# Performance work log

Measured on AMD Instinct MI355X. Metric: run time of the kernel, lower is better.

## Reference

```python
import jax, jax.numpy as jnp
import numpy as np

N = 5000        # nodes
F = 7699        # node feature dim (fixed by code)
E = 40000       # edges
ED = 3          # edge_dim (fixed by code)
H1, C1 = 4, 1024
H2, C2 = 1, 1024
NUM_OUT = 128
NEG_SLOPE = 0.2


def _glorot(key, shape):
    fan_in = shape[0]
    return jax.random.normal(key, shape, jnp.float32) / np.float32(np.sqrt(fan_in))


def setup_inputs() -> dict:
    key = jax.random.key(0)
    ks = jax.random.split(key, 16)
    x = jax.random.normal(ks[0], (N, F), jnp.float32)
    src = jax.random.randint(ks[1], (E,), 0, N)
    dst = jax.random.randint(ks[2], (E,), 0, N)
    src = jnp.where(src == dst, (src + 1) % N, src)  # no pre-existing self loops
    edge_index = jnp.stack([src, dst]).astype(jnp.int32)
    edge_attr = jax.random.normal(ks[3], (E, ED), jnp.float32)
    inp = {
        "x": x, "edge_index": edge_index, "edge_attr": edge_attr,
        # GATv2Conv #1: 7699 -> 1024, heads=4, edge_dim=3
        "W1l": _glorot(ks[4], (F, H1 * C1)), "b1l": jnp.zeros((H1 * C1,), jnp.float32),
        "W1r": _glorot(ks[5], (F, H1 * C1)), "b1r": jnp.zeros((H1 * C1,), jnp.float32),
        "W1e": _glorot(ks[6], (ED, H1 * C1)),
        "att1": _glorot(ks[7], (H1, C1)),
        "bias1": jnp.zeros((H1 * C1,), jnp.float32),
        # GATv2Conv #2: 4096 -> 1024, heads=1, edge_dim=3
        "W2l": _glorot(ks[8], (H1 * C1, H2 * C2)), "b2l": jnp.zeros((H2 * C2,), jnp.float32),
        "W2r": _glorot(ks[9], (H1 * C1, H2 * C2)), "b2r": jnp.zeros((H2 * C2,), jnp.float32),
        "W2e": _glorot(ks[10], (ED, H2 * C2)),
        "att2": _glorot(ks[11], (H2, C2)),
        "bias2": jnp.zeros((H2 * C2,), jnp.float32),
        # final Linear(1024, num_outputs)
        "Wlin": _glorot(ks[12], (C2, NUM_OUT)), "blin": jnp.zeros((NUM_OUT,), jnp.float32),
    }
    return inp


def gatv2_layer(x, src, dst, edge_attr, Wl, bl, Wr, br, We, att, bias, heads, out_ch):
    """PyG GATv2Conv with add_self_loops=True, fill_value='mean', concat=True."""
    n = x.shape[0]
    # self-loop edge_attr = mean of incoming edge attrs per node (fill_value='mean')
    deg = jax.ops.segment_sum(jnp.ones((src.shape[0],), jnp.float32), dst, num_segments=n)
    loop_attr = jax.ops.segment_sum(edge_attr, dst, num_segments=n) / jnp.maximum(deg, 1.0)[:, None]
    idx = jnp.arange(n, dtype=src.dtype)
    srcf = jnp.concatenate([src, idx])
    dstf = jnp.concatenate([dst, idx])
    ea = jnp.concatenate([edge_attr, loop_attr], axis=0)
    xl = (x @ Wl + bl).reshape(n, heads, out_ch)   # lin_l (source)
    xr = (x @ Wr + br).reshape(n, heads, out_ch)   # lin_r (target)
    ee = (ea @ We).reshape(-1, heads, out_ch)       # lin_edge (no bias)
    e = jax.nn.leaky_relu(xl[srcf] + xr[dstf] + ee, NEG_SLOPE)  # [E', H, C]
    logit = jnp.einsum('ehc,hc->eh', e, att)                     # [E', H]
    # segment softmax over destination nodes (every node has a self loop)
    m = jax.lax.stop_gradient(jax.ops.segment_max(logit, dstf, num_segments=n))
    a = jnp.exp(logit - m[dstf])
    denom = jax.ops.segment_sum(a, dstf, num_segments=n)
    alpha = a / (denom[dstf] + 1e-16)
    out = jax.ops.segment_sum(alpha[:, :, None] * xl[srcf], dstf, num_segments=n)  # [N,H,C]
    return out.reshape(n, heads * out_ch) + bias


def reference(x, edge_index, edge_attr,
              W1l, b1l, W1r, b1r, W1e, att1, bias1,
              W2l, b2l, W2r, b2r, W2e, att2, bias2,
              Wlin, blin):
    src, dst = edge_index[0], edge_index[1]
    h = gatv2_layer(x, src, dst, edge_attr, W1l, b1l, W1r, b1r, W1e, att1, bias1, H1, C1)
    h = gatv2_layer(h, src, dst, edge_attr, W2l, b2l, W2r, b2r, W2e, att2, bias2, H2, C2)
    return h @ Wlin + blin
```

## Files before the change

kernel.cpp:

```cpp
#include <hip/hip_runtime.h>
#include <cstdint>
#include <cstddef>

#define N_NODES 5000
#define F_IN    7699
#define KP1     7712
#define KT1     241
#define MP      5120
#define E_EDGES 40000
#define EFULL   45000
#define HC1     4096
#define N1      8192
#define HC2     1024
#define N2      2048
#define NOUT    128
#define GM      (MP / 256)

typedef __bf16 bf16x8 __attribute__((ext_vector_type(8)));
typedef float  f32x4  __attribute__((ext_vector_type(4)));
typedef float  f32x16 __attribute__((ext_vector_type(16)));
typedef unsigned short u16x8 __attribute__((ext_vector_type(8)));
typedef _Float16 f16;
typedef _Float16 f16x8 __attribute__((ext_vector_type(8)));

using as1_uchar = unsigned char __attribute__((address_space(1)));
using as3_uchar = unsigned char __attribute__((address_space(3)));

__device__ __forceinline__ unsigned short f2bf(float f) {
  union { float f; unsigned int u; } v; v.f = f;
  return (unsigned short)((v.u + 0x7fffu + ((v.u >> 16) & 1u)) >> 16);
}
__device__ __forceinline__ float bf2f(unsigned short h) {
  union { unsigned int u; float f; } v; v.u = ((unsigned int)h) << 16;
  return v.f;
}

__device__ __forceinline__ void gload16(const void* g, void* l) {
  __builtin_amdgcn_global_load_lds(
      reinterpret_cast<const as1_uchar*>(reinterpret_cast<uintptr_t>(g)),
      reinterpret_cast<as3_uchar*>(reinterpret_cast<uintptr_t>(l)),
      16, 0, 0);
}



__global__ void k_split_x(const float* __restrict__ x, unsigned short* __restrict__ hi,
                          unsigned short* __restrict__ lo) {
  const int C8 = KP1 / 8;
  int ci = blockIdx.x * 256 + threadIdx.x;
  if (ci >= MP * C8) return;
  int r = ci / C8, c8 = ci % C8;
  int c = c8 * 8;
  u16x8 hb, lb;
  #pragma unroll
  for (int j = 0; j < 8; ++j) {
    float v = 0.f;
    if (r < N_NODES && (c + j) < F_IN) v = x[(size_t)r * F_IN + c + j];
    unsigned short h = f2bf(v);
    hb[j] = h; lb[j] = f2bf(v - bf2f(h));
  }
  size_t off = ((size_t)((r >> 7) * KT1 + (c >> 5)) * 4 + ((c >> 3) & 3)) * 1024 + (r & 127) * 8;
  *(u16x8*)&hi[off] = hb;
  *(u16x8*)&lo[off] = lb;
}


__global__ void k_split_w(const float* __restrict__ W,
                          unsigned short* __restrict__ hi, unsigned short* __restrict__ lo,
                          int K, int Nsrc, int c0, int KT, int rowOffset) {
  __shared__ float tile[32][33];
  const int tid = threadIdx.x;
  const int kt = blockIdx.x;
  const int n0 = blockIdx.y * 32;
  #pragma unroll
  for (int i = tid >> 5; i < 32; i += 8) {
    int k = kt * 32 + i;
    tile[i][tid & 31] = (k < K) ? W[(size_t)k * Nsrc + c0 + n0 + (tid & 31)] : 0.f;
  }
  __syncthreads();
  if (tid < 128) {
    const int nn = tid >> 2, kc = (tid & 3) << 3;
    const int n = rowOffset + n0 + nn;
    u16x8 hb, lb;
    #pragma unroll
    for (int j = 0; j < 8; ++j) {
      float v = tile[kc + j][nn];
      unsigned short h = f2bf(v);
      hb[j] = h; lb[j] = f2bf(v - bf2f(h));
    }
    size_t off = ((size_t)((n >> 7) * KT + kt) * 4 + (kc >> 3)) * 1024 + (n & 127) * 8;
    *(u16x8*)&hi[off] = hb;
    *(u16x8*)&lo[off] = lb;
  }
}


template <int OF16>
__global__ __launch_bounds__(512, 2) void k_gemm_bb(
    const unsigned short* __restrict__ Ahi, const unsigned short* __restrict__ Alo,
    const unsigned short* __restrict__ Bhi, const unsigned short* __restrict__ Blo,
    void* __restrict__ Cp, const float* __restrict__ bias0, const float* __restrict__ bias1,
    int halfN, int M, int Nc, int ldC, int KT32, int nbn)
{
  __shared__ __align__(16) unsigned short S[3 * 16384];

  const int tid = threadIdx.x;
  const int lane = tid & 63;
  const int w = tid >> 6;
  const int wm = w >> 2, wn = w & 3;

  const int nwg = gridDim.x;
  const int qq = nwg >> 3, rr = nwg & 7;
  const int xcd = blockIdx.x & 7, idx = blockIdx.x >> 3;
  const int wg = (xcd < rr ? xcd * (qq + 1) : rr * (qq + 1) + (xcd - rr) * qq) + idx;
  const int bm = wg / nbn, bn = wg % nbn;

  f32x16 acc[4][2] = {};

  const int st = (w >> 2) & 1, sp = (w >> 1) & 1, sh = w & 1;
  const size_t laneoff = (size_t)sp * 1024 + sh * 512 + lane * 8;
  const unsigned short* gAh = Ahi + (size_t)(bm * 2 + st) * KT32 * 4096 + laneoff;
  const unsigned short* gAl = Alo + (size_t)(bm * 2 + st) * KT32 * 4096 + laneoff;
  const unsigned short* gBh = Bhi + (size_t)(bn * 2 + st) * KT32 * 4096 + laneoff;
  const unsigned short* gBl = Blo + (size_t)(bn * 2 + st) * KT32 * 4096 + laneoff;
  const int dA = (st * 2 + sp) * 1024 + sh * 512;

  auto stage = [&](int kt, int bufo) {
    const size_t o = (size_t)kt * 2048;
    gload16(gAh + o, &S[bufo + dA]);
    gload16(gAl + o, &S[bufo + 4096 + dA]);
    gload16(gBh + o, &S[bufo + 8192 + dA]);
    gload16(gBl + o, &S[bufo + 12288 + dA]);
  };

  const int r5 = lane & 31, h5 = lane >> 5;
  const int pA = (wm * 2 + h5) * 1024;
  const int pB = 8192 + ((wn >> 1) * 2 + h5) * 1024;
  int ra[4], cb[2];
  #pragma unroll
  for (int i = 0; i < 4; ++i) ra[i] = pA + (i * 32 + r5) * 8;
  #pragma unroll
  for (int j = 0; j < 2; ++j) cb[j] = pB + ((wn & 1) * 64 + j * 32 + r5) * 8;

  const int KT16 = KT32 * 2;

  stage(0, 0);
  stage(1, 16384);
  asm volatile("s_waitcnt vmcnt(4)" ::: "memory");
  __builtin_amdgcn_s_barrier();

  int ocur = 0, onxt = 16384, onx2 = 32768;
  for (int kt = 0; kt < KT16; ++kt) {
    const int ks = (kt + 2 < KT16) ? kt + 2 : KT16 - 1;
    stage(ks, onx2);

    bf16x8 ah[4], al[4], bh[2], bl[2];
    #pragma unroll
    for (int i = 0; i < 4; ++i) {
      ah[i] = *(const bf16x8*)&S[ocur + ra[i]];
      al[i] = *(const bf16x8*)&S[ocur + 4096 + ra[i]];
    }
    #pragma unroll
    for (int j = 0; j < 2; ++j) {
      bh[j] = *(const bf16x8*)&S[ocur + cb[j]];
      bl[j] = *(const bf16x8*)&S[ocur + 4096 + cb[j]];
    }

    __builtin_amdgcn_s_setprio(1);
    #pragma unroll
    for (int j = 0; j < 2; ++j)
      #pragma unroll
      for (int i = 0; i < 4; ++i) {
        acc[i][j] = __builtin_amdgcn_mfma_f32_32x32x16_bf16(ah[i], bh[j], acc[i][j], 0, 0, 0);
        acc[i][j] = __builtin_amdgcn_mfma_f32_32x32x16_bf16(al[i], bh[j], acc[i][j], 0, 0, 0);
        acc[i][j] = __builtin_amdgcn_mfma_f32_32x32x16_bf16(ah[i], bl[j], acc[i][j], 0, 0, 0);
      }
    __builtin_amdgcn_s_setprio(0);

    asm volatile("s_waitcnt vmcnt(4)" ::: "memory");
    __builtin_amdgcn_s_barrier();
    const int t = ocur; ocur = onxt; onxt = onx2; onx2 = t;
  }

  #pragma unroll
  for (int i = 0; i < 4; ++i) {
    #pragma unroll
    for (int j = 0; j < 2; ++j) {
      const int gc = bn * 256 + wn * 64 + j * 32 + r5;
      if (gc < Nc) {
        const float bv = (gc < halfN) ? bias0[gc] : bias1[gc - halfN];
        #pragma unroll
        for (int reg = 0; reg < 16; ++reg) {
          const int gr = bm * 256 + wm * 128 + i * 32 + (reg & 3) + 8 * (reg >> 2) + 4 * h5;
          if (gr < M) {
            float v = acc[i][j][reg] + bv;
            if (OF16) ((f16*)Cp)[(size_t)gr * ldC + gc] = (f16)v;
            else      ((float*)Cp)[(size_t)gr * ldC + gc] = v;
          }
        }
      }
    }
  }
}


__global__ void k_deg(const int* __restrict__ dst, const float* __restrict__ ea,
                      float* __restrict__ deg, float* __restrict__ lattr, int E) {
  int e = blockIdx.x * 256 + threadIdx.x;
  if (e >= E) return;
  int d = dst[e];
  atomicAdd(&deg[d], 1.f);
  atomicAdd(&lattr[d * 3 + 0], ea[e * 3 + 0]);
  atomicAdd(&lattr[d * 3 + 1], ea[e * 3 + 1]);
  atomicAdd(&lattr[d * 3 + 2], ea[e * 3 + 2]);
}

__global__ void k_lattr_fin(float* __restrict__ lattr, const float* __restrict__ deg, int n) {
  int i = blockIdx.x * 256 + threadIdx.x;
  if (i >= n) return;
  float dv = fmaxf(deg[i], 1.f);
  lattr[i * 3 + 0] /= dv; lattr[i * 3 + 1] /= dv; lattr[i * 3 + 2] /= dv;
}

__global__ void k_eafull(const float* __restrict__ ea, const float* __restrict__ lattr,
                         float* __restrict__ eaf, int E, int n) {
  int e = blockIdx.x * 256 + threadIdx.x;
  if (e >= E + n) return;
  const float* s = (e < E) ? &ea[(size_t)e * 3] : &lattr[(size_t)(e - E) * 3];
  eaf[e * 3 + 0] = s[0]; eaf[e * 3 + 1] = s[1]; eaf[e * 3 + 2] = s[2];
}

__global__ void k_count(const int* __restrict__ dst, int* __restrict__ cnt, int E, int n) {
  int e = blockIdx.x * 256 + threadIdx.x;
  if (e >= E + n) return;
  int d = (e < E) ? dst[e] : (e - E);
  atomicAdd(&cnt[d], 1);
}

__global__ void k_scan(const int* __restrict__ cnt, int* __restrict__ rowptr, int n) {
  int lane = threadIdx.x;
  int run = 0;
  for (int base = 0; base < n; base += 64) {
    int i = base + lane;
    int v = (i < n) ? cnt[i] : 0;
    #pragma unroll
    for (int off = 1; off < 64; off <<= 1) {
      int t = __shfl_up(v, off, 64);
      if (lane >= off) v += t;
    }
    if (i < n) rowptr[i + 1] = run + v;
    run += __shfl(v, 63, 64);
  }
  if (lane == 0) rowptr[0] = 0;
}

__global__ void k_fill(const int* __restrict__ dst, const int* __restrict__ rowptr,
                       int* __restrict__ fillc, int* __restrict__ elist, int E, int n) {
  int e = blockIdx.x * 256 + threadIdx.x;
  if (e >= E + n) return;
  int d = (e < E) ? dst[e] : (e - E);
  int pos = rowptr[d] + atomicAdd(&fillc[d], 1);
  elist[pos] = e;
}


template <int H, int ITERS>
__global__ __launch_bounds__(256) void k_logit(
    const f16* __restrict__ xl, const f16* __restrict__ xr, int strideX,
    const float* __restrict__ eaf, const float* __restrict__ We, const float* __restrict__ att,
    const int* __restrict__ src, const int* __restrict__ dst, int E,
    float* __restrict__ logit)
{
  const int e = blockIdx.x;
  const int tid = threadIdx.x;
  int s, d;
  if (e < E) { s = src[e]; d = dst[e]; } else { s = e - E; d = s; }
  const float ea0 = eaf[e * 3 + 0], ea1 = eaf[e * 3 + 1], ea2 = eaf[e * 3 + 2];
  constexpr int HC = ITERS * 256;
  const f16* rl = xl + (size_t)s * strideX;
  const f16* rr = xr + (size_t)d * strideX;
  float acc[H];
  #pragma unroll
  for (int h = 0; h < H; ++h) acc[h] = 0.f;
  #pragma unroll
  for (int i = 0; i < ITERS; ++i) {
    int hc = tid + (i << 8);
    float v = (float)rl[hc] + (float)rr[hc]
            + ea0 * We[hc] + ea1 * We[HC + hc] + ea2 * We[2 * HC + hc];
    v = (v > 0.f) ? v : 0.2f * v;
    acc[i >> 2] += v * att[hc];
  }
  __shared__ float red[H][4];
  const int lane = tid & 63, wv = tid >> 6;
  #pragma unroll
  for (int h = 0; h < H; ++h) {
    float v = acc[h];
    #pragma unroll
    for (int off = 32; off > 0; off >>= 1) v += __shfl_down(v, off, 64);
    if (lane == 0) red[h][wv] = v;
  }
  __syncthreads();
  if (tid < H)
    logit[(size_t)e * H + tid] = red[tid][0] + red[tid][1] + red[tid][2] + red[tid][3];
}

template <int H>
__global__ void k_stats(const float* __restrict__ logit, const int* __restrict__ rowptr,
                        const int* __restrict__ elist, float* __restrict__ mb, float* __restrict__ db)
{
  const int n = blockIdx.x;
  const int lane = threadIdx.x;
  const int start = rowptr[n], end = rowptr[n + 1];
  #pragma unroll
  for (int h = 0; h < H; ++h) {
    float m = -1e30f;
    for (int p = start + lane; p < end; p += 64)
      m = fmaxf(m, logit[(size_t)elist[p] * H + h]);
    #pragma unroll
    for (int off = 32; off > 0; off >>= 1) m = fmaxf(m, __shfl_down(m, off, 64));
    m = __shfl(m, 0, 64);
    float sum = 0.f;
    for (int p = start + lane; p < end; p += 64)
      sum += __expf(logit[(size_t)elist[p] * H + h] - m);
    #pragma unroll
    for (int off = 32; off > 0; off >>= 1) sum += __shfl_down(sum, off, 64);
    if (lane == 0) { mb[n * H + h] = m; db[n * H + h] = sum; }
  }
}

template <int H, int NC8, int KTo>
__global__ __launch_bounds__(256) void k_agg(
    const f16* __restrict__ xl, int strideX,
    const int* __restrict__ rowptr, const int* __restrict__ elist, const int* __restrict__ src,
    const float* __restrict__ logit, const float* __restrict__ mb, const float* __restrict__ db,
    const float* __restrict__ bias,
    unsigned short* __restrict__ ohi, unsigned short* __restrict__ olo, int E)
{
  const int n = blockIdx.x;
  const int tid = threadIdx.x;
  constexpr int HC = H * 1024;
  float acc[NC8][8];
  #pragma unroll
  for (int q = 0; q < NC8; ++q)
    #pragma unroll
    for (int j = 0; j < 8; ++j) acc[q][j] = 0.f;
  const int start = rowptr[n], end = rowptr[n + 1];
  float mloc[H], dloc[H];
  #pragma unroll
  for (int h = 0; h < H; ++h) { mloc[h] = mb[n * H + h]; dloc[h] = db[n * H + h] + 1e-16f; }
  for (int p = start; p < end; ++p) {
    const int e = elist[p];
    const int s = (e < E) ? src[e] : (e - E);
    float al[H];
    #pragma unroll
    for (int h = 0; h < H; ++h)
      al[h] = __expf(logit[(size_t)e * H + h] - mloc[h]) / dloc[h];
    const f16* row = xl + (size_t)s * strideX;
    #pragma unroll
    for (int q = 0; q < NC8; ++q) {
      const int c8 = tid + q * 256;
      if (c8 * 8 < HC) {
        float a = (H == 4) ? ((tid & 128) ? al[2 * q + 1] : al[2 * q]) : al[0];
        f16x8 v = *(const f16x8*)(row + c8 * 8);
        #pragma unroll
        for (int j = 0; j < 8; ++j) acc[q][j] += a * (float)v[j];
      }
    }
  }
  #pragma unroll
  for (int q = 0; q < NC8; ++q) {
    const int c8 = tid + q * 256;
    if (c8 * 8 < HC) {
      u16x8 hb, lb;
      #pragma unroll
      for (int j = 0; j < 8; ++j) {
        float v = acc[q][j] + bias[c8 * 8 + j];
        unsigned short h = f2bf(v);
        hb[j] = h; lb[j] = f2bf(v - bf2f(h));
      }
      size_t off = ((size_t)((n >> 7) * KTo + (c8 >> 2)) * 4 + (c8 & 3)) * 1024 + (n & 127) * 8;
      *(u16x8*)&ohi[off] = hb;
      *(u16x8*)&olo[off] = lb;
    }
  }
}


extern "C" void kernel_launch(void* const* d_in, const int* in_sizes, int n_in,
                              void* d_out, int out_size, void* d_ws, size_t ws_size,
                              hipStream_t stream) {
  const float* x    = (const float*)d_in[0];
  const int*   eidx = (const int*)d_in[1];
  const float* eattr= (const float*)d_in[2];
  const float* W1l  = (const float*)d_in[3];
  const float* b1l  = (const float*)d_in[4];
  const float* W1r  = (const float*)d_in[5];
  const float* b1r  = (const float*)d_in[6];
  const float* W1e  = (const float*)d_in[7];
  const float* att1 = (const float*)d_in[8];
  const float* bias1= (const float*)d_in[9];
  const float* W2l  = (const float*)d_in[10];
  const float* b2l  = (const float*)d_in[11];
  const float* W2r  = (const float*)d_in[12];
  const float* b2r  = (const float*)d_in[13];
  const float* W2e  = (const float*)d_in[14];
  const float* att2 = (const float*)d_in[15];
  const float* bias2= (const float*)d_in[16];
  const float* Wlin = (const float*)d_in[17];
  const float* blin = (const float*)d_in[18];
  float* out = (float*)d_out;

  char* ws = (char*)d_ws;
  const int* srcp = eidx;
  const int* dstp = eidx + E_EDGES;

  auto alignup = [](size_t v) { return (v + 255) & ~(size_t)255; };

  size_t mo = 0;
  auto take = [&](size_t sz) { size_t r = mo; mo = alignup(mo + sz); return r; };
  const size_t oLATTR = take((size_t)N_NODES * 3 * 4);
  const size_t oDEG   = take((size_t)N_NODES * 4);
  const size_t oEAF   = take((size_t)EFULL * 3 * 4);
  const size_t oCNT   = take((size_t)N_NODES * 4);
  const size_t oROW   = take((size_t)(N_NODES + 1) * 4);
  const size_t oFILL  = take((size_t)N_NODES * 4);
  const size_t oELIST = take((size_t)EFULL * 4);
  const size_t oLOGIT = take((size_t)EFULL * 4 * 4);
  const size_t oMB    = take((size_t)N_NODES * 4 * 4);
  const size_t oDB    = take((size_t)N_NODES * 4 * 4);
  const size_t oXHI   = take((size_t)MP * KP1 * 2);
  const size_t oXLO   = take((size_t)MP * KP1 * 2);
  const size_t oXLR   = take((size_t)N_NODES * N1 * 2);
  const size_t oBH    = take((size_t)N1 * KP1 * 2);
  const size_t oBL    = take((size_t)N1 * KP1 * 2);
  if (ws_size < mo) return;

  const size_t oH1HI = oXHI;
  const size_t oH1LO = oXLO;
  const size_t oXLR2 = oXLR;
  const size_t oH2HI = oXLR + 32ull * 1024 * 1024;
  const size_t oH2LO = oXLR + 48ull * 1024 * 1024;
  const size_t oB2H  = oBH;
  const size_t oB2L  = oBH + 32ull * 1024 * 1024;
  const size_t oB3H  = oBH;
  const size_t oB3L  = oBH + 1ull * 1024 * 1024;

  unsigned short* XHI  = (unsigned short*)(ws + oXHI);
  unsigned short* XLO  = (unsigned short*)(ws + oXLO);
  f16*            XLR  = (f16*)(ws + oXLR);
  unsigned short* BH   = (unsigned short*)(ws + oBH);
  unsigned short* BL   = (unsigned short*)(ws + oBL);
  float*          LATTR= (float*)(ws + oLATTR);
  float*          DEG  = (float*)(ws + oDEG);
  float*          EAF  = (float*)(ws + oEAF);
  int*            CNT  = (int*)(ws + oCNT);
  int*            ROWP = (int*)(ws + oROW);
  int*            FILLC= (int*)(ws + oFILL);
  int*            ELIST= (int*)(ws + oELIST);
  float*          LOGIT= (float*)(ws + oLOGIT);
  float*          MB   = (float*)(ws + oMB);
  float*          DB   = (float*)(ws + oDB);
  unsigned short* H1HI = (unsigned short*)(ws + oH1HI);
  unsigned short* H1LO = (unsigned short*)(ws + oH1LO);
  f16*            XLR2 = (f16*)(ws + oXLR2);
  unsigned short* H2HI = (unsigned short*)(ws + oH2HI);
  unsigned short* H2LO = (unsigned short*)(ws + oH2LO);
  unsigned short* B2H  = (unsigned short*)(ws + oB2H);
  unsigned short* B2L  = (unsigned short*)(ws + oB2L);
  unsigned short* B3H  = (unsigned short*)(ws + oB3H);
  unsigned short* B3L  = (unsigned short*)(ws + oB3L);

  hipMemsetAsync(ws + oDEG,   0, (size_t)N_NODES * 4, stream);
  hipMemsetAsync(ws + oLATTR, 0, (size_t)N_NODES * 3 * 4, stream);
  hipMemsetAsync(ws + oCNT,   0, (size_t)N_NODES * 4, stream);
  hipMemsetAsync(ws + oFILL,  0, (size_t)N_NODES * 4, stream);

  const int gE  = (E_EDGES + 255) / 256;
  const int gEF = (EFULL + 255) / 256;
  const int gN  = (N_NODES + 255) / 256;

  k_deg<<<gE, 256, 0, stream>>>(dstp, eattr, DEG, LATTR, E_EDGES);
  k_lattr_fin<<<gN, 256, 0, stream>>>(LATTR, DEG, N_NODES);
  k_eafull<<<gEF, 256, 0, stream>>>(eattr, LATTR, EAF, E_EDGES, N_NODES);
  k_count<<<gEF, 256, 0, stream>>>(dstp, CNT, E_EDGES, N_NODES);
  k_scan<<<1, 64, 0, stream>>>(CNT, ROWP, N_NODES);
  k_fill<<<gEF, 256, 0, stream>>>(dstp, ROWP, FILLC, ELIST, E_EDGES, N_NODES);

  k_split_x<<<MP * (KP1 / 8) / 256, 256, 0, stream>>>(x, XHI, XLO);
  k_split_w<<<dim3(KT1, HC1 / 32), 256, 0, stream>>>(W1l, BH, BL, F_IN, HC1, 0, KT1, 0);
  k_split_w<<<dim3(KT1, HC1 / 32), 256, 0, stream>>>(W1r, BH, BL, F_IN, HC1, 0, KT1, HC1);
  k_gemm_bb<1><<<GM * (N1 / 256), 512, 0, stream>>>(
      XHI, XLO, BH, BL, XLR, b1l, b1r, HC1, N_NODES, N1, N1, KT1, N1 / 256);

  k_logit<4, 16><<<EFULL, 256, 0, stream>>>(XLR, XLR + HC1, N1, EAF, W1e, att1, srcp, dstp, E_EDGES, LOGIT);
  k_stats<4><<<N_NODES, 64, 0, stream>>>(LOGIT, ROWP, ELIST, MB, DB);
  hipMemsetAsync(ws + oH1HI, 0, (size_t)MP * HC1 * 2, stream);
  hipMemsetAsync(ws + oH1LO, 0, (size_t)MP * HC1 * 2, stream);
  k_agg<4, 2, HC1 / 32><<<N_NODES, 256, 0, stream>>>(
      XLR, N1, ROWP, ELIST, srcp, LOGIT, MB, DB, bias1, H1HI, H1LO, E_EDGES);

  k_split_w<<<dim3(HC1 / 32, HC2 / 32), 256, 0, stream>>>(W2l, B2H, B2L, HC1, HC2, 0, HC1 / 32, 0);
  k_split_w<<<dim3(HC1 / 32, HC2 / 32), 256, 0, stream>>>(W2r, B2H, B2L, HC1, HC2, 0, HC1 / 32, HC2);
  k_gemm_bb<1><<<GM * (N2 / 256), 512, 0, stream>>>(
      H1HI, H1LO, B2H, B2L, XLR2, b2l, b2r, HC2, N_NODES, N2, N2, HC1 / 32, N2 / 256);

  k_logit<1, 4><<<EFULL, 256, 0, stream>>>(XLR2, XLR2 + HC2, N2, EAF, W2e, att2, srcp, dstp, E_EDGES, LOGIT);
  k_stats<1><<<N_NODES, 64, 0, stream>>>(LOGIT, ROWP, ELIST, MB, DB);
  hipMemsetAsync(ws + oH2HI, 0, (size_t)MP * HC2 * 2, stream);
  hipMemsetAsync(ws + oH2LO, 0, (size_t)MP * HC2 * 2, stream);
  k_agg<1, 1, HC2 / 32><<<N_NODES, 256, 0, stream>>>(
      XLR2, N2, ROWP, ELIST, srcp, LOGIT, MB, DB, bias2, H2HI, H2LO, E_EDGES);

  hipMemsetAsync(ws + oB3H, 0, (size_t)2 * 32 * 4096 * 2, stream);
  hipMemsetAsync(ws + oB3L, 0, (size_t)2 * 32 * 4096 * 2, stream);
  k_split_w<<<dim3(HC2 / 32, NOUT / 32), 256, 0, stream>>>(Wlin, B3H, B3L, HC2, NOUT, 0, HC2 / 32, 0);
  k_gemm_bb<0><<<GM * 1, 512, 0, stream>>>(
      H2HI, H2LO, B3H, B3L, out, blin, blin, NOUT, N_NODES, NOUT, NOUT, HC2 / 32, 1);
}
```

Measured before the change: 2.886 ms.

## Restructure bf16x3 GEMM to 4 waves with 128x128 per-wave tiles

The split-bf16 GEMM goes from 8 waves (512 threads, each computing a 128x64 sub-tile) to 4 waves (256 threads, each computing 128x128). The 256x256 block tile and the 3-stage LDS pipeline stay the same. Each wave now issues 8 async global loads per stage instead of 4, and the vmcnt waits are adjusted to match. Larger per-wave tiles raise MFMA work per LDS fragment load, but they double the accumulator registers to 256 fp32 per lane. Occupancy also drops to one 4-wave block per CU, which risks weaker latency hiding.

```diff
diff --git a/kernel.cpp b/kernel.cpp
--- a/kernel.cpp
+++ b/kernel.cpp
@@ -96,7 +96,7 @@
 
 
 template <int OF16>
-__global__ __launch_bounds__(512, 2) void k_gemm_bb(
+__global__ __launch_bounds__(256, 1) void k_gemm_bb(
     const unsigned short* __restrict__ Ahi, const unsigned short* __restrict__ Alo,
     const unsigned short* __restrict__ Bhi, const unsigned short* __restrict__ Blo,
     void* __restrict__ Cp, const float* __restrict__ bias0, const float* __restrict__ bias1,
@@ -107,7 +107,7 @@
   const int tid = threadIdx.x;
   const int lane = tid & 63;
   const int w = tid >> 6;
-  const int wm = w >> 2, wn = w & 3;
+  const int wm = w >> 1, wn = w & 1;
 
   const int nwg = gridDim.x;
   const int qq = nwg >> 3, rr = nwg & 7;
@@ -115,38 +115,37 @@
   const int wg = (xcd < rr ? xcd * (qq + 1) : rr * (qq + 1) + (xcd - rr) * qq) + idx;
   const int bm = wg / nbn, bn = wg % nbn;
 
-  f32x16 acc[4][2] = {};
-
-  const int st = (w >> 2) & 1, sp = (w >> 1) & 1, sh = w & 1;
-  const size_t laneoff = (size_t)sp * 1024 + sh * 512 + lane * 8;
-  const unsigned short* gAh = Ahi + (size_t)(bm * 2 + st) * KT32 * 4096 + laneoff;
-  const unsigned short* gAl = Alo + (size_t)(bm * 2 + st) * KT32 * 4096 + laneoff;
-  const unsigned short* gBh = Bhi + (size_t)(bn * 2 + st) * KT32 * 4096 + laneoff;
-  const unsigned short* gBl = Blo + (size_t)(bn * 2 + st) * KT32 * 4096 + laneoff;
-  const int dA = (st * 2 + sp) * 1024 + sh * 512;
-
-  auto stage = [&](int kt, int bufo) {
-    const size_t o = (size_t)kt * 2048;
-    gload16(gAh + o, &S[bufo + dA]);
-    gload16(gAl + o, &S[bufo + 4096 + dA]);
-    gload16(gBh + o, &S[bufo + 8192 + dA]);
-    gload16(gBl + o, &S[bufo + 12288 + dA]);
+  f32x16 acc[4][4] = {};
+
+  const unsigned short* gbase = (w == 0) ? Ahi : (w == 1) ? Alo : (w == 2) ? Bhi : Blo;
+  const int brow = (w < 2) ? bm * 2 : bn * 2;
+  const unsigned short* gsrc[8];
+  int dd[8];
+  #pragma unroll
+  for (int d = 0; d < 8; ++d) {
+    const int t = d >> 2, p = (d >> 1) & 1, hf = d & 1;
+    gsrc[d] = gbase + (size_t)(brow + t) * KT32 * 4096 + p * 1024 + hf * 512 + lane * 8;
+    dd[d] = w * 4096 + t * 2048 + p * 1024 + hf * 512;
+  }
+
+  auto stage = [&](int kt16, int bufo) {
+    const size_t o = (size_t)kt16 * 2048;
+    #pragma unroll
+    for (int d = 0; d < 8; ++d) gload16(gsrc[d] + o, &S[bufo + dd[d]]);
   };
 
   const int r5 = lane & 31, h5 = lane >> 5;
-  const int pA = (wm * 2 + h5) * 1024;
-  const int pB = 8192 + ((wn >> 1) * 2 + h5) * 1024;
-  int ra[4], cb[2];
-  #pragma unroll
-  for (int i = 0; i < 4; ++i) ra[i] = pA + (i * 32 + r5) * 8;
-  #pragma unroll
-  for (int j = 0; j < 2; ++j) cb[j] = pB + ((wn & 1) * 64 + j * 32 + r5) * 8;
+  int ra[4], cb[4];
+  #pragma unroll
+  for (int i = 0; i < 4; ++i) ra[i] = wm * 2048 + h5 * 1024 + (i * 32 + r5) * 8;
+  #pragma unroll
+  for (int j = 0; j < 4; ++j) cb[j] = 8192 + wn * 2048 + h5 * 1024 + (j * 32 + r5) * 8;
 
   const int KT16 = KT32 * 2;
 
   stage(0, 0);
   stage(1, 16384);
-  asm volatile("s_waitcnt vmcnt(4)" ::: "memory");
+  asm volatile("s_waitcnt vmcnt(8)" ::: "memory");
   __builtin_amdgcn_s_barrier();
 
   int ocur = 0, onxt = 16384, onx2 = 32768;
@@ -154,21 +153,21 @@
     const int ks = (kt + 2 < KT16) ? kt + 2 : KT16 - 1;
     stage(ks, onx2);
 
-    bf16x8 ah[4], al[4], bh[2], bl[2];
+    bf16x8 ah[4], al[4], bh[4], bl[4];
     #pragma unroll
     for (int i = 0; i < 4; ++i) {
       ah[i] = *(const bf16x8*)&S[ocur + ra[i]];
       al[i] = *(const bf16x8*)&S[ocur + 4096 + ra[i]];
     }
     #pragma unroll
-    for (int j = 0; j < 2; ++j) {
+    for (int j = 0; j < 4; ++j) {
       bh[j] = *(const bf16x8*)&S[ocur + cb[j]];
       bl[j] = *(const bf16x8*)&S[ocur + 4096 + cb[j]];
     }
 
     __builtin_amdgcn_s_setprio(1);
     #pragma unroll
-    for (int j = 0; j < 2; ++j)
+    for (int j = 0; j < 4; ++j)
       #pragma unroll
       for (int i = 0; i < 4; ++i) {
         acc[i][j] = __builtin_amdgcn_mfma_f32_32x32x16_bf16(ah[i], bh[j], acc[i][j], 0, 0, 0);
@@ -177,7 +176,7 @@
       }
     __builtin_amdgcn_s_setprio(0);
 
-    asm volatile("s_waitcnt vmcnt(4)" ::: "memory");
+    asm volatile("s_waitcnt vmcnt(8)" ::: "memory");
     __builtin_amdgcn_s_barrier();
     const int t = ocur; ocur = onxt; onxt = onx2; onx2 = t;
   }
@@ -185,8 +184,8 @@
   #pragma unroll
   for (int i = 0; i < 4; ++i) {
     #pragma unroll
-    for (int j = 0; j < 2; ++j) {
-      const int gc = bn * 256 + wn * 64 + j * 32 + r5;
+    for (int j = 0; j < 4; ++j) {
+      const int gc = bn * 256 + wn * 128 + j * 32 + r5;
       if (gc < Nc) {
         const float bv = (gc < halfN) ? bias0[gc] : bias1[gc - halfN];
         #pragma unroll
@@ -489,7 +488,7 @@
   k_split_x<<<MP * (KP1 / 8) / 256, 256, 0, stream>>>(x, XHI, XLO);
   k_split_w<<<dim3(KT1, HC1 / 32), 256, 0, stream>>>(W1l, BH, BL, F_IN, HC1, 0, KT1, 0);
   k_split_w<<<dim3(KT1, HC1 / 32), 256, 0, stream>>>(W1r, BH, BL, F_IN, HC1, 0, KT1, HC1);
-  k_gemm_bb<1><<<GM * (N1 / 256), 512, 0, stream>>>(
+  k_gemm_bb<1><<<GM * (N1 / 256), 256, 0, stream>>>(
       XHI, XLO, BH, BL, XLR, b1l, b1r, HC1, N_NODES, N1, N1, KT1, N1 / 256);
 
   k_logit<4, 16><<<EFULL, 256, 0, stream>>>(XLR, XLR + HC1, N1, EAF, W1e, att1, srcp, dstp, E_EDGES, LOGIT);
@@ -501,7 +500,7 @@
 
   k_split_w<<<dim3(HC1 / 32, HC2 / 32), 256, 0, stream>>>(W2l, B2H, B2L, HC1, HC2, 0, HC1 / 32, 0);
   k_split_w<<<dim3(HC1 / 32, HC2 / 32), 256, 0, stream>>>(W2r, B2H, B2L, HC1, HC2, 0, HC1 / 32, HC2);
-  k_gemm_bb<1><<<GM * (N2 / 256), 512, 0, stream>>>(
+  k_gemm_bb<1><<<GM * (N2 / 256), 256, 0, stream>>>(
       H1HI, H1LO, B2H, B2L, XLR2, b2l, b2r, HC2, N_NODES, N2, N2, HC1 / 32, N2 / 256);
 
   k_logit<1, 4><<<EFULL, 256, 0, stream>>>(XLR2, XLR2 + HC2, N2, EAF, W2e, att2, srcp, dstp, E_EDGES, LOGIT);
@@ -514,6 +513,6 @@
   hipMemsetAsync(ws + oB3H, 0, (size_t)2 * 32 * 4096 * 2, stream);
   hipMemsetAsync(ws + oB3L, 0, (size_t)2 * 32 * 4096 * 2, stream);
   k_split_w<<<dim3(HC2 / 32, NOUT / 32), 256, 0, stream>>>(Wlin, B3H, B3L, HC2, NOUT, 0, HC2 / 32, 0);
-  k_gemm_bb<0><<<GM * 1, 512, 0, stream>>>(
+  k_gemm_bb<0><<<GM * 1, 256, 0, stream>>>(
       H2HI, H2LO, B3H, B3L, out, blin, blin, NOUT, N_NODES, NOUT, NOUT, HC2 / 32, 1);
 }
```

After: 3.003 ms. +4.1%, slower.

## Deepen GEMM LDS pipeline to four stages with register-prefetched fragments

Applied to the files above, without the earlier changes.

The bf16 split-precision GEMM moves from a 3-buffer to a 4-buffer LDS ring and unrolls the k-loop by two. It reads the next tile's fragments into a second register set before issuing MFMAs on the current set, so LDS reads overlap matrix work. Global loads are remapped so each wave issues four loads per stage across Ahi/Alo/Bhi/Blo. The trade-off is 128 KB of LDS per block, which likely prevents two blocks per CU despite the launch bounds, and doubling the fragment registers raises register pressure.

```diff
diff --git a/kernel.cpp b/kernel.cpp
--- a/kernel.cpp
+++ b/kernel.cpp
@@ -102,7 +102,7 @@
     void* __restrict__ Cp, const float* __restrict__ bias0, const float* __restrict__ bias1,
     int halfN, int M, int Nc, int ldC, int KT32, int nbn)
 {
-  __shared__ __align__(16) unsigned short S[3 * 16384];
+  __shared__ __align__(16) unsigned short S[4 * 16384];
 
   const int tid = threadIdx.x;
   const int lane = tid & 63;
@@ -117,69 +117,82 @@
 
   f32x16 acc[4][2] = {};
 
-  const int st = (w >> 2) & 1, sp = (w >> 1) & 1, sh = w & 1;
-  const size_t laneoff = (size_t)sp * 1024 + sh * 512 + lane * 8;
-  const unsigned short* gAh = Ahi + (size_t)(bm * 2 + st) * KT32 * 4096 + laneoff;
-  const unsigned short* gAl = Alo + (size_t)(bm * 2 + st) * KT32 * 4096 + laneoff;
-  const unsigned short* gBh = Bhi + (size_t)(bn * 2 + st) * KT32 * 4096 + laneoff;
-  const unsigned short* gBl = Blo + (size_t)(bn * 2 + st) * KT32 * 4096 + laneoff;
-  const int dA = (st * 2 + sp) * 1024 + sh * 512;
-
-  auto stage = [&](int kt, int bufo) {
-    const size_t o = (size_t)kt * 2048;
-    gload16(gAh + o, &S[bufo + dA]);
-    gload16(gAl + o, &S[bufo + 4096 + dA]);
-    gload16(gBh + o, &S[bufo + 8192 + dA]);
-    gload16(gBl + o, &S[bufo + 12288 + dA]);
+  const unsigned short* gsrc[4];
+  int dd[4];
+  #pragma unroll
+  for (int s = 0; s < 4; ++s) {
+    const int q = w * 4 + s;
+    const int r_ = q & 7, t = r_ >> 2, p = (r_ >> 1) & 1, hf = r_ & 1;
+    const unsigned short* base = (q < 8) ? Ahi : (q < 16) ? Alo : (q < 24) ? Bhi : Blo;
+    const int brow = ((q < 16) ? bm : bn) * 2 + t;
+    gsrc[s] = base + (size_t)brow * KT32 * 4096 + p * 1024 + hf * 512 + lane * 8;
+    dd[s] = (q >> 3) * 4096 + t * 2048 + p * 1024 + hf * 512;
+  }
+
+  auto stage = [&](int kt16, int bufo) {
+    const size_t o = (size_t)kt16 * 2048;
+    #pragma unroll
+    for (int s = 0; s < 4; ++s) gload16(gsrc[s] + o, &S[bufo + dd[s]]);
   };
 
   const int r5 = lane & 31, h5 = lane >> 5;
-  const int pA = (wm * 2 + h5) * 1024;
-  const int pB = 8192 + ((wn >> 1) * 2 + h5) * 1024;
   int ra[4], cb[2];
   #pragma unroll
-  for (int i = 0; i < 4; ++i) ra[i] = pA + (i * 32 + r5) * 8;
-  #pragma unroll
-  for (int j = 0; j < 2; ++j) cb[j] = pB + ((wn & 1) * 64 + j * 32 + r5) * 8;
-
-  const int KT16 = KT32 * 2;
-
-  stage(0, 0);
-  stage(1, 16384);
-  asm volatile("s_waitcnt vmcnt(4)" ::: "memory");
-  __builtin_amdgcn_s_barrier();
-
-  int ocur = 0, onxt = 16384, onx2 = 32768;
-  for (int kt = 0; kt < KT16; ++kt) {
-    const int ks = (kt + 2 < KT16) ? kt + 2 : KT16 - 1;
-    stage(ks, onx2);
-
-    bf16x8 ah[4], al[4], bh[2], bl[2];
+  for (int i = 0; i < 4; ++i) ra[i] = wm * 2048 + h5 * 1024 + (i * 32 + r5) * 8;
+  #pragma unroll
+  for (int j = 0; j < 2; ++j)
+    cb[j] = 8192 + (wn >> 1) * 2048 + h5 * 1024 + ((wn & 1) * 64 + j * 32 + r5) * 8;
+
+  struct Frags { bf16x8 ah[4], al[4], bh[2], bl[2]; };
+  auto rdfr = [&](Frags& f, int bufo) {
     #pragma unroll
     for (int i = 0; i < 4; ++i) {
-      ah[i] = *(const bf16x8*)&S[ocur + ra[i]];
-      al[i] = *(const bf16x8*)&S[ocur + 4096 + ra[i]];
+      f.ah[i] = *(const bf16x8*)&S[bufo + ra[i]];
+      f.al[i] = *(const bf16x8*)&S[bufo + 4096 + ra[i]];
     }
     #pragma unroll
     for (int j = 0; j < 2; ++j) {
-      bh[j] = *(const bf16x8*)&S[ocur + cb[j]];
-      bl[j] = *(const bf16x8*)&S[ocur + 4096 + cb[j]];
-    }
-
+      f.bh[j] = *(const bf16x8*)&S[bufo + cb[j]];
+      f.bl[j] = *(const bf16x8*)&S[bufo + 4096 + cb[j]];
+    }
+  };
+  auto domfma = [&](Frags& f) {
     __builtin_amdgcn_s_setprio(1);
     #pragma unroll
     for (int j = 0; j < 2; ++j)
       #pragma unroll
       for (int i = 0; i < 4; ++i) {
-        acc[i][j] = __builtin_amdgcn_mfma_f32_32x32x16_bf16(ah[i], bh[j], acc[i][j], 0, 0, 0);
-        acc[i][j] = __builtin_amdgcn_mfma_f32_32x32x16_bf16(al[i], bh[j], acc[i][j], 0, 0, 0);
-        acc[i][j] = __builtin_amdgcn_mfma_f32_32x32x16_bf16(ah[i], bl[j], acc[i][j], 0, 0, 0);
+        acc[i][j] = __builtin_amdgcn_mfma_f32_32x32x16_bf16(f.ah[i], f.bh[j], acc[i][j], 0, 0, 0);
+        acc[i][j] = __builtin_amdgcn_mfma_f32_32x32x16_bf16(f.al[i], f.bh[j], acc[i][j], 0, 0, 0);
+        acc[i][j] = __builtin_amdgcn_mfma_f32_32x32x16_bf16(f.ah[i], f.bl[j], acc[i][j], 0, 0, 0);
       }
     __builtin_amdgcn_s_setprio(0);
-
+  };
+
+  const int KT16 = KT32 * 2;
+
+  stage(0, 0);
+  stage(1, 16384);
+  stage(2, 32768);
+  asm volatile("s_waitcnt vmcnt(4)" ::: "memory");
+  __builtin_amdgcn_s_barrier();
+  Frags fA, fB;
+  rdfr(fA, 0);
+
+  int o0 = 0, o1 = 16384, o2 = 32768, o3 = 49152;
+  for (int kt = 0; kt < KT16; kt += 2) {
+    stage((kt + 3 < KT16) ? kt + 3 : KT16 - 1, o3);
+    rdfr(fB, o1);
+    domfma(fA);
     asm volatile("s_waitcnt vmcnt(4)" ::: "memory");
     __builtin_amdgcn_s_barrier();
-    const int t = ocur; ocur = onxt; onxt = onx2; onx2 = t;
+    stage((kt + 4 < KT16) ? kt + 4 : KT16 - 1, o0);
+    rdfr(fA, o2);
+    domfma(fB);
+    asm volatile("s_waitcnt vmcnt(4)" ::: "memory");
+    __builtin_amdgcn_s_barrier();
+    int t0 = o0, t1 = o1;
+    o0 = o2; o1 = o3; o2 = t0; o3 = t1;
   }
 
   #pragma unroll
```

Result: faster. 2.807 ms (-2.7%).
